# Kernel optimization log

Hardware: AMD Instinct MI355X
Metric: run time of the kernel (lower is better)

The kernel has to match this reference:

```python
import jax, jax.numpy as jnp
import numpy as np

B, S, D, H = 2, 2048, 1024, 16
DH = D // H  # 64


def setup_inputs() -> dict:
    key = jax.random.key(0)
    ks = jax.random.split(key, 12)
    scale = 0.02
    q = jax.random.normal(ks[0], (B, S, D), dtype=jnp.float32)
    k = jax.random.normal(ks[1], (B, S, D), dtype=jnp.float32)
    v = jax.random.normal(ks[2], (B, S, D), dtype=jnp.float32)
    # CTRL-style causal mask: 1.0 above the diagonal (positions to mask), 0.0 elsewhere
    mask = jnp.triu(jnp.ones((S, S), dtype=jnp.float32), k=1)
    Wq = jax.random.normal(ks[3], (D, D), dtype=jnp.float32) * scale
    bq = jnp.zeros((D,), dtype=jnp.float32)
    Wk = jax.random.normal(ks[4], (D, D), dtype=jnp.float32) * scale
    bk = jnp.zeros((D,), dtype=jnp.float32)
    Wv = jax.random.normal(ks[5], (D, D), dtype=jnp.float32) * scale
    bv = jnp.zeros((D,), dtype=jnp.float32)
    Wo = jax.random.normal(ks[6], (D, D), dtype=jnp.float32) * scale
    bo = jnp.zeros((D,), dtype=jnp.float32)
    return {"q": q, "k": k, "v": v, "mask": mask,
            "Wq": Wq, "bq": bq, "Wk": Wk, "bk": bk,
            "Wv": Wv, "bv": bv, "Wo": Wo, "bo": bo}


def _split_heads(x):
    # [B, S, D] -> [B, H, S, DH]
    b, s, _ = x.shape
    return x.reshape(b, s, H, DH).transpose(0, 2, 1, 3)


def reference(q, k, v, mask, Wq, bq, Wk, bk, Wv, bv, Wo, bo):
    # QKV projections
    qh = _split_heads(q @ Wq + bq)  # [B, H, S, DH]
    kh = _split_heads(k @ Wk + bk)
    vh = _split_heads(v @ Wv + bv)
    # scaled dot-product attention with CTRL mask convention (mask * -1e4 added)
    scores = jnp.einsum('bhqd,bhkd->bhqk', qh, kh) / jnp.sqrt(jnp.float32(DH))
    scores = scores + mask * -10000.0  # mask broadcasts [S,S] -> [B,H,S,S]
    weights = jax.nn.softmax(scores, axis=-1)
    ctx = jnp.einsum('bhqk,bhkd->bhqd', weights, vh)  # [B, H, S, DH]
    ctx = ctx.transpose(0, 2, 1, 3).reshape(q.shape[0], -1, D)  # [B, S, D]
    return ctx @ Wo + bo
```

## Files before the change

kernel.cpp:

```cpp
#include <hip/hip_runtime.h>
#include <stdint.h>

typedef unsigned short u16;
typedef __attribute__((ext_vector_type(8))) short bf16x8;
typedef __attribute__((ext_vector_type(4))) float f32x4;
typedef __attribute__((ext_vector_type(4))) unsigned short u16x4;

#define C_SCALE 0.1803368801111204f
#define C_MASK  -14426.950408889634f

__device__ __forceinline__ float bf2f(u16 x) {
  union { uint32_t u; float f; } v; v.u = ((uint32_t)x) << 16; return v.f;
}
__device__ __forceinline__ u16 f2bf(float f) {
  union { float f; uint32_t u; } v; v.f = f;
  return (u16)((v.u + 0x7FFFu + ((v.u >> 16) & 1u)) >> 16);
}

__device__ __forceinline__ void load_lds16(const void* g, void* l) {
  __builtin_amdgcn_global_load_lds(
      (const __attribute__((address_space(1))) uint32_t*)g,
      (__attribute__((address_space(3))) uint32_t*)l, 16, 0, 0);
}

__device__ __forceinline__ uint32_t pack_trunc(uint32_t f_even, uint32_t f_odd) {
  return __builtin_amdgcn_perm(f_odd, f_even, 0x07060302u);
}

__device__ __forceinline__ bool detect_bf16(const u16* __restrict__ q) {
  int lane = threadIdx.x & 63;
  u16 w = q[lane * 4];
  int e = (w >> 7) & 0xFF;
  unsigned long long b = __ballot(e >= 96 && e <= 159);
  return __popcll(b) >= 48;
}

__global__ __launch_bounds__(256) void transpose_all(const u16* __restrict__ W0,
                                                     const u16* __restrict__ W1,
                                                     const u16* __restrict__ W2,
                                                     const u16* __restrict__ W3,
                                                     u16* __restrict__ WTb,
                                                     const u16* __restrict__ qprobe) {
  constexpr int D = 1024;
  __shared__ u16 tile[64][72];
  const int z = blockIdx.z;
  const u16* W = z == 0 ? W0 : (z == 1 ? W1 : (z == 2 ? W2 : W3));
  u16* WT = WTb + (size_t)z * D * D;
  const bool isbf = detect_bf16(qprobe);
  const int x0 = blockIdx.x * 64, y0 = blockIdx.y * 64;
  const int t = threadIdx.x;
  const int r = t >> 3;
  const int c8 = (t & 7) << 3;
#pragma unroll
  for (int hh = 0; hh < 2; ++hh) {
    int row = r + hh * 32;
    if (isbf) {
      *(uint4*)&tile[row][c8] = *(const uint4*)&W[(size_t)(y0 + row) * D + x0 + c8];
    } else {
      const float* Wf = (const float*)W;
      float4 f0 = *(const float4*)&Wf[(size_t)(y0 + row) * D + x0 + c8];
      float4 f1 = *(const float4*)&Wf[(size_t)(y0 + row) * D + x0 + c8 + 4];
      u16 tmp[8] = {f2bf(f0.x), f2bf(f0.y), f2bf(f0.z), f2bf(f0.w),
                    f2bf(f1.x), f2bf(f1.y), f2bf(f1.z), f2bf(f1.w)};
      *(uint4*)&tile[row][c8] = *(uint4*)tmp;
    }
  }
  __syncthreads();
#pragma unroll
  for (int hh = 0; hh < 2; ++hh) {
    int row = r + hh * 32;
    u16 tmp[8];
#pragma unroll
    for (int i = 0; i < 8; ++i) tmp[i] = tile[c8 + i][row];
    *(uint4*)&WT[(size_t)(x0 + row) * D + y0 + c8] = *(uint4*)tmp;
  }
}

__global__ __launch_bounds__(256, 2) void gemm_qkv(
    const u16* __restrict__ A0, const u16* __restrict__ A1, const u16* __restrict__ A2,
    const u16* __restrict__ WTb,
    const u16* __restrict__ b0, const u16* __restrict__ b1, const u16* __restrict__ b2,
    u16* __restrict__ Chb) {
  constexpr int K = 1024;
  __shared__ u16 As[4][64 * 40];
  __shared__ u16 Bs[4][128 * 32];
  const int z = blockIdx.z;
  const u16* A = z == 0 ? A0 : (z == 1 ? A1 : A2);
  const u16* bias = z == 0 ? b0 : (z == 1 ? b1 : b2);
  const u16* BT = WTb + (size_t)z * 1024 * 1024;
  u16* C = Chb + (size_t)z * 4 * 1024 * 1024;
  const bool isbf = detect_bf16(A0);
  const int tid = threadIdx.x;
  const int wave = tid >> 6, lane = tid & 63;
  const int quad = lane >> 4, lr = lane & 15;
  const int f = blockIdx.x + 8 * blockIdx.y;
  const int n0 = (f >> 6) * 128;
  const int m0 = (f & 63) * 64;
  const int mW = (wave & 1) * 32, nW = (wave >> 1) * 64;
  const int ar = tid >> 2, ac = tid & 3;

  uint4 ra[2][2];
  auto loadA = [&](int t) {
    int slot = t & 1, k0 = t * 32;
    if (isbf) {
      ra[slot][0] = *(const uint4*)&A[(size_t)(m0 + ar) * K + k0 + ac * 8];
    } else {
      const uint32_t* Af = (const uint32_t*)A;
      ra[slot][0] = *(const uint4*)&Af[(size_t)(m0 + ar) * K + k0 + ac * 8];
      ra[slot][1] = *(const uint4*)&Af[(size_t)(m0 + ar) * K + k0 + ac * 8 + 4];
    }
  };
  auto writeA = [&](int t) {
    int slot = t & 1, buf = t & 3;
    if (isbf) {
      *(uint4*)&As[buf][ar * 40 + ac * 8] = ra[slot][0];
    } else {
      uint4 o;
      o.x = pack_trunc(ra[slot][0].x, ra[slot][0].y);
      o.y = pack_trunc(ra[slot][0].z, ra[slot][0].w);
      o.z = pack_trunc(ra[slot][1].x, ra[slot][1].y);
      o.w = pack_trunc(ra[slot][1].z, ra[slot][1].w);
      *(uint4*)&As[buf][ar * 40 + ac * 8] = o;
    }
  };
  auto stageB = [&](int t) {
    int buf = t & 3, k0 = t * 32;
#pragma unroll
    for (int p = 0; p < 2; ++p) {
      int s = (wave * 2 + p) * 64 + lane;
      int r = s >> 2, c = s & 3;
      int cg = c ^ (r & 3);
      load_lds16(&BT[(size_t)(n0 + r) * K + k0 + cg * 8],
                 &Bs[buf][(wave * 2 + p) * 512]);
    }
  };

  f32x4 acc[2][4] = {};

  loadA(0); loadA(1);
  stageB(0); stageB(1);
  writeA(0); writeA(1);
  loadA(2); loadA(3);
  __syncthreads();

  for (int j = 0; j < 16; ++j) {
    const int tc0 = 2 * j, tc1 = 2 * j + 1;
    if (tc0 + 2 < 32) {
      writeA(tc0 + 2); writeA(tc1 + 2);
      stageB(tc0 + 2); stageB(tc1 + 2);
      if (tc0 + 4 < 32) { loadA(tc0 + 4); loadA(tc1 + 4); }
    }
#pragma unroll
    for (int tt = 0; tt < 2; ++tt) {
      const int buf = (tc0 + tt) & 3;
      bf16x8 af[2], bfm[4];
#pragma unroll
      for (int i = 0; i < 2; ++i)
        af[i] = *(const bf16x8*)&As[buf][(mW + 16 * i + lr) * 40 + quad * 8];
#pragma unroll
      for (int jj = 0; jj < 4; ++jj) {
        int rr = nW + 16 * jj + lr;
        bfm[jj] = *(const bf16x8*)&Bs[buf][rr * 32 + ((quad ^ (rr & 3)) * 8)];
      }
#pragma unroll
      for (int i = 0; i < 2; ++i)
#pragma unroll
        for (int jj = 0; jj < 4; ++jj)
          acc[i][jj] =
              __builtin_amdgcn_mfma_f32_16x16x32_bf16(af[i], bfm[jj], acc[i][jj], 0, 0, 0);
    }
    __syncthreads();
  }

#pragma unroll
  for (int i = 0; i < 2; ++i) {
#pragma unroll
    for (int jj = 0; jj < 4; ++jj) {
      int n = n0 + nW + 16 * jj + lr;
      float bv = isbf ? bf2f(bias[n]) : ((const float*)bias)[n];
#pragma unroll
      for (int r = 0; r < 4; ++r) {
        int m = m0 + mW + 16 * i + quad * 4 + r;
        float val = acc[i][jj][r] + bv;
        int b = m >> 11, s = m & 2047, h = n >> 6, dh = n & 63;
        C[((size_t)(b * 16 + h) * 2048 + s) * 64 + dh] = f2bf(val);
      }
    }
  }
}

__global__ __launch_bounds__(256, 2) void gemm_out(const u16* __restrict__ A,
                                                   const u16* __restrict__ BT,
                                                   const u16* __restrict__ bias,
                                                   u16* __restrict__ C,
                                                   const u16* __restrict__ qprobe) {
  constexpr int K = 1024, N = 1024;
  __shared__ u16 As[4][64 * 32];
  __shared__ u16 Bs[4][128 * 32];
  const bool isbf = detect_bf16(qprobe);
  const int tid = threadIdx.x;
  const int wave = tid >> 6, lane = tid & 63;
  const int quad = lane >> 4, lr = lane & 15;
  const int f = blockIdx.x + 8 * blockIdx.y;
  const int n0 = (f >> 6) * 128;
  const int m0 = (f & 63) * 64;
  const int mW = (wave & 1) * 32, nW = (wave >> 1) * 64;

  auto stage = [&](int t) {
    int buf = t & 3, k0 = t * 32;
    {
      int s = wave * 64 + lane;
      int r = s >> 2, c = s & 3;
      int cg = c ^ (r & 3);
      load_lds16(&A[(size_t)(m0 + r) * K + k0 + cg * 8], &As[buf][wave * 512]);
    }
#pragma unroll
    for (int p = 0; p < 2; ++p) {
      int s = (wave * 2 + p) * 64 + lane;
      int r = s >> 2, c = s & 3;
      int cg = c ^ (r & 3);
      load_lds16(&BT[(size_t)(n0 + r) * K + k0 + cg * 8],
                 &Bs[buf][(wave * 2 + p) * 512]);
    }
  };

  f32x4 acc[2][4] = {};
  stage(0); stage(1);
  __syncthreads();

  for (int j = 0; j < 16; ++j) {
    const int tc0 = 2 * j;
    if (tc0 + 2 < 32) { stage(tc0 + 2); stage(tc0 + 3); }
#pragma unroll
    for (int tt = 0; tt < 2; ++tt) {
      const int buf = (tc0 + tt) & 3;
      bf16x8 af[2], bfm[4];
#pragma unroll
      for (int i = 0; i < 2; ++i) {
        int rr = mW + 16 * i + lr;
        af[i] = *(const bf16x8*)&As[buf][rr * 32 + ((quad ^ (rr & 3)) * 8)];
      }
#pragma unroll
      for (int jj = 0; jj < 4; ++jj) {
        int rr = nW + 16 * jj + lr;
        bfm[jj] = *(const bf16x8*)&Bs[buf][rr * 32 + ((quad ^ (rr & 3)) * 8)];
      }
#pragma unroll
      for (int i = 0; i < 2; ++i)
#pragma unroll
        for (int jj = 0; jj < 4; ++jj)
          acc[i][jj] =
              __builtin_amdgcn_mfma_f32_16x16x32_bf16(af[i], bfm[jj], acc[i][jj], 0, 0, 0);
    }
    __syncthreads();
  }

#pragma unroll
  for (int i = 0; i < 2; ++i) {
#pragma unroll
    for (int jj = 0; jj < 4; ++jj) {
      int n = n0 + nW + 16 * jj + lr;
      float bv = isbf ? bf2f(bias[n]) : ((const float*)bias)[n];
#pragma unroll
      for (int r = 0; r < 4; ++r) {
        int m = m0 + mW + 16 * i + quad * 4 + r;
        float val = acc[i][jj][r] + bv;
        size_t idx = (size_t)m * N + n;
        if (isbf) C[idx] = f2bf(val);
        else ((float*)C)[idx] = val;
      }
    }
  }
}

__global__ __launch_bounds__(256, 2) void attn_fwd(const u16* __restrict__ Qh,
                                                   const u16* __restrict__ Kh,
                                                   const u16* __restrict__ Vh,
                                                   u16* __restrict__ ctx) {
  constexpr int S = 2048, DH = 64, Dm = 1024;
  __shared__ u16 Ks[2][64 * 64];
  __shared__ u16 Vt[2][64 * 72];
  __shared__ u16 Pl[4][16 * 72];
  const int tid = threadIdx.x;
  const int wave = tid >> 6, lane = tid & 63;
  const int quad = lane >> 4, lr = lane & 15;
  const int bh = blockIdx.y;
  const int bx = (int)blockIdx.x;
  const size_t base = (size_t)bh * S * DH;
  const u16* Q = Qh + base;
  const u16* Kp = Kh + base;
  const u16* Vp = Vh + base;
  u16* Plw = Pl[wave];
  const int b = bh >> 4, h = bh & 15;

  const int vkey2 = (tid & 31) * 2, vd8 = (tid >> 5) * 8;
  uint4 va, vbr;

  auto stageK = [&](int kt, int kbuf) {
#pragma unroll
    for (int p = 0; p < 2; ++p) {
      int s = (wave * 2 + p) * 64 + lane;
      int r = s >> 3, cg = (s & 7) ^ (r & 7);
      load_lds16(&Kp[(size_t)(kt + r) * DH + cg * 8], &Ks[kbuf][(wave * 2 + p) * 512]);
    }
  };
  auto loadV = [&](int kt) {
    va  = *(const uint4*)&Vp[(size_t)(kt + vkey2) * DH + vd8];
    vbr = *(const uint4*)&Vp[(size_t)(kt + vkey2 + 1) * DH + vd8];
  };
  auto writeV = [&](int vbuf) {
    const u16* pa = (const u16*)&va;
    const u16* pb = (const u16*)&vbr;
#pragma unroll
    for (int i = 0; i < 8; ++i) {
      uint32_t pair = (uint32_t)pa[i] | ((uint32_t)pb[i] << 16);
      *(uint32_t*)&Vt[vbuf][(vd8 + i) * 72 + vkey2] = pair;
    }
  };

  int kb = 0, vb = 0;
  for (int ph = 0; ph < 2; ++ph) {
    const int qt = ph == 0 ? (31 - bx) : bx;
    const int q0 = qt * 64;
    const int nt = qt + 1;
    const int qg = q0 + wave * 16 + lr;

    bf16x8 aQ[2];
#pragma unroll
    for (int s = 0; s < 2; ++s)
      aQ[s] = *(const bf16x8*)&Q[(size_t)(q0 + wave * 16 + lr) * DH + s * 32 + quad * 8];

    f32x4 o[4] = {};
    float m_i = -1.0e5f;
    float l_i = 0.f;

    __syncthreads();
    stageK(0, kb);
    loadV(0);
    writeV(vb);
    if (nt > 1) loadV(64);

    for (int it = 0; it < nt; ++it) {
      const int kt = it * 64;
      __syncthreads();

      bf16x8 aK[4][2], bV[4][2];
#pragma unroll
      for (int t = 0; t < 4; ++t) {
        int r = t * 16 + lr;
#pragma unroll
        for (int s = 0; s < 2; ++s) {
          int ch = (s * 4 + quad) ^ (r & 7);
          aK[t][s] = *(const bf16x8*)&Ks[kb][r * 64 + ch * 8];
        }
      }
#pragma unroll
      for (int c = 0; c < 4; ++c)
#pragma unroll
        for (int s = 0; s < 2; ++s)
          bV[c][s] = *(const bf16x8*)&Vt[vb][(c * 16 + lr) * 72 + s * 32 + quad * 8];

      if (it + 1 < nt) {
        stageK(kt + 64, kb ^ 1);
        writeV(vb ^ 1);
        if (it + 2 < nt) loadV(kt + 128);
      }

      f32x4 sc[4];
#pragma unroll
      for (int t = 0; t < 4; ++t) {
        f32x4 zz = {0.f, 0.f, 0.f, 0.f};
        zz = __builtin_amdgcn_mfma_f32_16x16x32_bf16(aK[t][0], aQ[0], zz, 0, 0, 0);
        zz = __builtin_amdgcn_mfma_f32_16x16x32_bf16(aK[t][1], aQ[1], zz, 0, 0, 0);
        sc[t] = zz;
      }

      const bool diag = (it == nt - 1);
      float v[4][4];
      float mx = -1.0e5f;
      if (diag) {
#pragma unroll
        for (int t = 0; t < 4; ++t)
#pragma unroll
          for (int r = 0; r < 4; ++r) {
            int kg = kt + t * 16 + quad * 4 + r;
            float x = sc[t][r] * C_SCALE + ((kg > qg) ? C_MASK : 0.f);
            v[t][r] = x;
            mx = fmaxf(mx, x);
          }
      } else {
#pragma unroll
        for (int t = 0; t < 4; ++t)
#pragma unroll
          for (int r = 0; r < 4; ++r) {
            float x = sc[t][r] * C_SCALE;
            v[t][r] = x;
            mx = fmaxf(mx, x);
          }
      }
      mx = fmaxf(mx, __shfl_xor(mx, 16));
      mx = fmaxf(mx, __shfl_xor(mx, 32));
      float m_new = fmaxf(m_i, mx);
      float sum = 0.f;
      u16 pb16[4][4];
#pragma unroll
      for (int t = 0; t < 4; ++t)
#pragma unroll
        for (int r = 0; r < 4; ++r) {
          float p = exp2f(v[t][r] - m_new);
          sum += p;
          pb16[t][r] = f2bf(p);
        }
      sum += __shfl_xor(sum, 16);
      sum += __shfl_xor(sum, 32);
      float alpha = exp2f(m_i - m_new);
      l_i = l_i * alpha + sum;
      m_i = m_new;
#pragma unroll
      for (int t = 0; t < 4; ++t) {
        u16x4 w = {pb16[t][0], pb16[t][1], pb16[t][2], pb16[t][3]};
        *(u16x4*)&Plw[lr * 72 + t * 16 + quad * 4] = w;
      }
#pragma unroll
      for (int r = 0; r < 4; ++r) {
        float ab = __shfl(alpha, quad * 4 + r);
#pragma unroll
        for (int c = 0; c < 4; ++c) o[c][r] *= ab;
      }
      asm volatile("s_waitcnt lgkmcnt(0)" ::: "memory");
      bf16x8 aP[2];
#pragma unroll
      for (int s = 0; s < 2; ++s)
        aP[s] = *(const bf16x8*)&Plw[lr * 72 + s * 32 + quad * 8];
#pragma unroll
      for (int c = 0; c < 4; ++c)
#pragma unroll
        for (int s = 0; s < 2; ++s)
          o[c] = __builtin_amdgcn_mfma_f32_16x16x32_bf16(aP[s], bV[c][s], o[c], 0, 0, 0);
      kb ^= 1; vb ^= 1;
    }

    float linv = 1.f / l_i;
#pragma unroll
    for (int r = 0; r < 4; ++r) {
      float lb = __shfl(linv, quad * 4 + r);
      int s = q0 + wave * 16 + quad * 4 + r;
      size_t orow = ((size_t)b * S + s) * Dm + h * DH;
#pragma unroll
      for (int c = 0; c < 4; ++c) ctx[orow + c * 16 + lr] = f2bf(o[c][r] * lb);
    }
  }
}

extern "C" void kernel_launch(void* const* d_in, const int* in_sizes, int n_in,
                              void* d_out, int out_size, void* d_ws, size_t ws_size,
                              hipStream_t stream) {
  const u16* q  = (const u16*)d_in[0];
  const u16* k  = (const u16*)d_in[1];
  const u16* v  = (const u16*)d_in[2];
  const u16* Wq = (const u16*)d_in[4];
  const u16* bq = (const u16*)d_in[5];
  const u16* Wk = (const u16*)d_in[6];
  const u16* bk = (const u16*)d_in[7];
  const u16* Wv = (const u16*)d_in[8];
  const u16* bv = (const u16*)d_in[9];
  const u16* Wo = (const u16*)d_in[10];
  const u16* bo = (const u16*)d_in[11];
  u16* out = (u16*)d_out;

  constexpr size_t M1 = 1024 * 1024;
  u16* ws = (u16*)d_ws;
  u16* WT  = ws;
  u16* Qh  = WT + 4 * M1;
  u16* ctx = Qh + 12 * M1;

  dim3 tb(256);
  transpose_all<<<dim3(16, 16, 4), tb, 0, stream>>>(Wq, Wk, Wv, Wo, WT, q);
  gemm_qkv<<<dim3(8, 64, 3), tb, 0, stream>>>(q, k, v, WT, bq, bk, bv, Qh);
  attn_fwd<<<dim3(16, 32), tb, 0, stream>>>(Qh, Qh + 4 * M1, Qh + 8 * M1, ctx);
  gemm_out<<<dim3(8, 64), tb, 0, stream>>>(ctx, WT + 3 * M1, bo, out, q);
}
```

Before: 252.2 us.

## Rework projection GEMMs with 128x128 tiles and explicit multi-stage waitcnt pipelines

Both the QKV and output projection GEMMs move from 64x128 to 128x128 block tiles, so each wave now computes a 64x64 sub-tile with 16 MFMAs per k-step. The k-loop is rewritten as an N-stage ring buffer, 3 stages for QKV and 6 for the output GEMM, driven by manual s_waitcnt vmcnt counts, raw s_barrier and sched_barrier instead of __syncthreads. This is meant to raise data reuse per LDS read and keep global loads overlapping with compute. It adds a separate fp32-input path that converts A through registers, and it reduces the grid to 256 blocks per GEMM, which costs occupancy and relies on hand-tuned wait counts being correct.

```diff
diff --git a/kernel.cpp b/kernel.cpp
--- a/kernel.cpp
+++ b/kernel.cpp
@@ -34,6 +34,22 @@
   unsigned long long b = __ballot(e >= 96 && e <= 159);
   return __popcll(b) >= 48;
 }
+
+__device__ __forceinline__ void wait_vm(int n) {
+  switch (n) {
+    case 0:  __builtin_amdgcn_s_waitcnt(0x0F70); break;
+    case 2:  __builtin_amdgcn_s_waitcnt(0x0F72); break;
+    case 4:  __builtin_amdgcn_s_waitcnt(0x0F74); break;
+    case 6:  __builtin_amdgcn_s_waitcnt(0x0F76); break;
+    case 8:  __builtin_amdgcn_s_waitcnt(0x0F78); break;
+    case 12: __builtin_amdgcn_s_waitcnt(0x0F7C); break;
+    case 16: __builtin_amdgcn_s_waitcnt(0x4F70); break;
+    default: __builtin_amdgcn_s_waitcnt(0x4F74); break;
+  }
+}
+__device__ __forceinline__ void wait_lgkm0() { __builtin_amdgcn_s_waitcnt(0xC07F); }
+#define SBAR()  __builtin_amdgcn_s_barrier()
+#define SCHED() __builtin_amdgcn_sched_barrier(0)
 
 __global__ __launch_bounds__(256) void transpose_all(const u16* __restrict__ W0,
                                                      const u16* __restrict__ W1,
@@ -76,15 +92,177 @@
   }
 }
 
-__global__ __launch_bounds__(256, 2) void gemm_qkv(
+
+__device__ __forceinline__ void stage_tile32(const u16* __restrict__ src, int row0,
+                                             int k0, u16* dst, int wave, int lane) {
+  constexpr int K = 1024;
+#pragma unroll
+  for (int p = 0; p < 2; ++p) {
+    int seg = wave * 2 + p;
+    int r = seg * 16 + (lane >> 2);
+    int c = lane & 3;
+    int cg = c ^ (r & 3);
+    load_lds16(&src[(size_t)(row0 + r) * K + k0 + cg * 8], dst + seg * 512);
+  }
+}
+
+#define FRAG_READS(Ab, Bb)                                                    \
+  _Pragma("unroll") for (int i = 0; i < 4; ++i) {                             \
+    int r = wm + 16 * i + lr;                                                 \
+    af[i] = *(const bf16x8*)&(Ab)[r * 32 + ((quad ^ (r & 3)) * 8)];           \
+  }                                                                           \
+  _Pragma("unroll") for (int jj = 0; jj < 4; ++jj) {                          \
+    int r = wn + 16 * jj + lr;                                                \
+    bff[jj] = *(const bf16x8*)&(Bb)[r * 32 + ((quad ^ (r & 3)) * 8)];         \
+  }
+
+#define MFMA16()                                                              \
+  _Pragma("unroll") for (int i = 0; i < 4; ++i)                               \
+  _Pragma("unroll") for (int jj = 0; jj < 4; ++jj)                            \
+      acc[i][jj] = __builtin_amdgcn_mfma_f32_16x16x32_bf16(af[i], bff[jj],    \
+                                                           acc[i][jj], 0, 0, 0);
+
+template <int NS>
+__device__ __forceinline__ void kloop_dma(const u16* __restrict__ A,
+                                          const u16* __restrict__ BT,
+                                          int m0, int n0, u16* As, u16* Bs,
+                                          int wave, int lane, f32x4 (&acc)[4][4]) {
+  const int quad = lane >> 4, lr = lane & 15;
+  const int wm = (wave & 1) * 64, wn = (wave >> 1) * 64;
+  auto stage = [&](int t, int buf) {
+    stage_tile32(A, m0, t * 32, As + buf * 4096, wave, lane);
+    stage_tile32(BT, n0, t * 32, Bs + buf * 4096, wave, lane);
+  };
+#pragma unroll
+  for (int s = 0; s < NS; ++s) stage(s, s);
+  int buf = 0;
+#pragma unroll 1
+  for (int t = 0; t < 32; ++t) {
+    SCHED();
+    int rem = 31 - t;
+    wait_vm(rem >= NS - 1 ? 4 * (NS - 1) : 4 * rem);
+    SBAR();
+    SCHED();
+    bf16x8 af[4], bff[4];
+    const u16* Ab = As + buf * 4096;
+    const u16* Bb = Bs + buf * 4096;
+    FRAG_READS(Ab, Bb)
+    wait_lgkm0();
+    SCHED();
+    SBAR();
+    if (t + NS < 32) stage(t + NS, buf);
+    MFMA16()
+    buf = buf + 1 == NS ? 0 : buf + 1;
+  }
+}
+
+__device__ __forceinline__ void kloop_f32(const float* __restrict__ Af,
+                                          const u16* __restrict__ BT,
+                                          int m0, int n0, u16* As, u16* Bs,
+                                          int tid, f32x4 (&acc)[4][4]) {
+  constexpr int K = 1024;
+  const int wave = tid >> 6, lane = tid & 63;
+  const int quad = lane >> 4, lr = lane & 15;
+  const int wm = (wave & 1) * 64, wn = (wave >> 1) * 64;
+  const int ar = tid >> 1, ah = tid & 1;
+  const uint32_t* Au = (const uint32_t*)Af;
+  uint4 ra0[4], ra1[4];
+  auto loadA = [&](int t, uint4 (&r)[4]) {
+    const uint32_t* p = &Au[(size_t)(m0 + ar) * K + t * 32 + ah * 16];
+    r[0] = *(const uint4*)(p + 0);
+    r[1] = *(const uint4*)(p + 4);
+    r[2] = *(const uint4*)(p + 8);
+    r[3] = *(const uint4*)(p + 12);
+  };
+  auto writeA = [&](int buf, uint4 (&rr)[4]) {
+    uint4 o0, o1;
+    o0.x = pack_trunc(rr[0].x, rr[0].y); o0.y = pack_trunc(rr[0].z, rr[0].w);
+    o0.z = pack_trunc(rr[1].x, rr[1].y); o0.w = pack_trunc(rr[1].z, rr[1].w);
+    o1.x = pack_trunc(rr[2].x, rr[2].y); o1.y = pack_trunc(rr[2].z, rr[2].w);
+    o1.z = pack_trunc(rr[3].x, rr[3].y); o1.w = pack_trunc(rr[3].z, rr[3].w);
+    int c0 = 2 * ah, c1 = 2 * ah + 1;
+    *(uint4*)&As[buf * 4096 + ar * 32 + ((c0 ^ (ar & 3)) * 8)] = o0;
+    *(uint4*)&As[buf * 4096 + ar * 32 + ((c1 ^ (ar & 3)) * 8)] = o1;
+  };
+  auto stageB = [&](int t, int buf) {
+    stage_tile32(BT, n0, t * 32, Bs + buf * 4096, wave, lane);
+  };
+  stageB(0, 0); loadA(0, ra0);
+  stageB(1, 1); loadA(1, ra1);
+  SCHED(); wait_vm(6); writeA(0, ra0);
+  stageB(2, 2); loadA(2, ra0);
+  SCHED(); wait_vm(6); writeA(1, ra1);
+  loadA(3, ra1);
+  SCHED(); wait_vm(4); writeA(2, ra0);
+
+  int buf = 0;
+#pragma unroll 1
+  for (int j = 0; j < 14; ++j) {
+#pragma unroll
+    for (int half = 0; half < 2; ++half) {
+      const int t = 2 * j + half;
+      SCHED();
+      wait_vm(16);
+      SBAR();
+      SCHED();
+      bf16x8 af[4], bff[4];
+      const u16* Ab = As + buf * 4096;
+      const u16* Bb = Bs + buf * 4096;
+      FRAG_READS(Ab, Bb)
+      wait_lgkm0();
+      SCHED();
+      SBAR();
+      stageB(t + 3, buf);
+      if (half == 0) { loadA(t + 4, ra0); SCHED(); wait_vm(6); writeA(buf, ra1); }
+      else           { loadA(t + 4, ra1); SCHED(); wait_vm(6); writeA(buf, ra0); }
+      MFMA16()
+      buf = buf + 1 == 3 ? 0 : buf + 1;
+    }
+  }
+  {
+    SCHED(); wait_vm(16); SBAR(); SCHED();
+    bf16x8 af[4], bff[4];
+    const u16 *Ab = As + buf * 4096, *Bb = Bs + buf * 4096;
+    FRAG_READS(Ab, Bb)
+    wait_lgkm0(); SCHED(); SBAR();
+    stageB(31, buf);
+    SCHED(); wait_vm(2); writeA(buf, ra1);
+    MFMA16()
+    buf = 2;
+  }
+  {
+    SCHED(); wait_vm(12); SBAR(); SCHED();
+    bf16x8 af[4], bff[4];
+    const u16 *Ab = As + buf * 4096, *Bb = Bs + buf * 4096;
+    FRAG_READS(Ab, Bb)
+    MFMA16()
+    buf = 0;
+  }
+  {
+    SCHED(); wait_vm(6); SBAR(); SCHED();
+    bf16x8 af[4], bff[4];
+    const u16 *Ab = As + buf * 4096, *Bb = Bs + buf * 4096;
+    FRAG_READS(Ab, Bb)
+    MFMA16()
+    buf = 1;
+  }
+  {
+    SCHED(); wait_vm(0); SBAR(); SCHED();
+    bf16x8 af[4], bff[4];
+    const u16 *Ab = As + buf * 4096, *Bb = Bs + buf * 4096;
+    FRAG_READS(Ab, Bb)
+    MFMA16()
+  }
+}
+
+__global__ __launch_bounds__(256, 3) void gemm_qkv(
     const u16* __restrict__ A0, const u16* __restrict__ A1, const u16* __restrict__ A2,
     const u16* __restrict__ WTb,
     const u16* __restrict__ b0, const u16* __restrict__ b1, const u16* __restrict__ b2,
     u16* __restrict__ Chb) {
-  constexpr int K = 1024;
-  __shared__ u16 As[4][64 * 40];
-  __shared__ u16 Bs[4][128 * 32];
-  const int z = blockIdx.z;
+  __shared__ u16 As[3 * 4096];
+  __shared__ u16 Bs[3 * 4096];
+  const int z = blockIdx.y;
   const u16* A = z == 0 ? A0 : (z == 1 ? A1 : A2);
   const u16* bias = z == 0 ? b0 : (z == 1 ? b1 : b2);
   const u16* BT = WTb + (size_t)z * 1024 * 1024;
@@ -93,94 +271,24 @@
   const int tid = threadIdx.x;
   const int wave = tid >> 6, lane = tid & 63;
   const int quad = lane >> 4, lr = lane & 15;
-  const int f = blockIdx.x + 8 * blockIdx.y;
-  const int n0 = (f >> 6) * 128;
-  const int m0 = (f & 63) * 64;
-  const int mW = (wave & 1) * 32, nW = (wave >> 1) * 64;
-  const int ar = tid >> 2, ac = tid & 3;
-
-  uint4 ra[2][2];
-  auto loadA = [&](int t) {
-    int slot = t & 1, k0 = t * 32;
-    if (isbf) {
-      ra[slot][0] = *(const uint4*)&A[(size_t)(m0 + ar) * K + k0 + ac * 8];
-    } else {
-      const uint32_t* Af = (const uint32_t*)A;
-      ra[slot][0] = *(const uint4*)&Af[(size_t)(m0 + ar) * K + k0 + ac * 8];
-      ra[slot][1] = *(const uint4*)&Af[(size_t)(m0 + ar) * K + k0 + ac * 8 + 4];
-    }
-  };
-  auto writeA = [&](int t) {
-    int slot = t & 1, buf = t & 3;
-    if (isbf) {
-      *(uint4*)&As[buf][ar * 40 + ac * 8] = ra[slot][0];
-    } else {
-      uint4 o;
-      o.x = pack_trunc(ra[slot][0].x, ra[slot][0].y);
-      o.y = pack_trunc(ra[slot][0].z, ra[slot][0].w);
-      o.z = pack_trunc(ra[slot][1].x, ra[slot][1].y);
-      o.w = pack_trunc(ra[slot][1].z, ra[slot][1].w);
-      *(uint4*)&As[buf][ar * 40 + ac * 8] = o;
-    }
-  };
-  auto stageB = [&](int t) {
-    int buf = t & 3, k0 = t * 32;
-#pragma unroll
-    for (int p = 0; p < 2; ++p) {
-      int s = (wave * 2 + p) * 64 + lane;
-      int r = s >> 2, c = s & 3;
-      int cg = c ^ (r & 3);
-      load_lds16(&BT[(size_t)(n0 + r) * K + k0 + cg * 8],
-                 &Bs[buf][(wave * 2 + p) * 512]);
-    }
-  };
-
-  f32x4 acc[2][4] = {};
-
-  loadA(0); loadA(1);
-  stageB(0); stageB(1);
-  writeA(0); writeA(1);
-  loadA(2); loadA(3);
-  __syncthreads();
-
-  for (int j = 0; j < 16; ++j) {
-    const int tc0 = 2 * j, tc1 = 2 * j + 1;
-    if (tc0 + 2 < 32) {
-      writeA(tc0 + 2); writeA(tc1 + 2);
-      stageB(tc0 + 2); stageB(tc1 + 2);
-      if (tc0 + 4 < 32) { loadA(tc0 + 4); loadA(tc1 + 4); }
-    }
-#pragma unroll
-    for (int tt = 0; tt < 2; ++tt) {
-      const int buf = (tc0 + tt) & 3;
-      bf16x8 af[2], bfm[4];
-#pragma unroll
-      for (int i = 0; i < 2; ++i)
-        af[i] = *(const bf16x8*)&As[buf][(mW + 16 * i + lr) * 40 + quad * 8];
-#pragma unroll
-      for (int jj = 0; jj < 4; ++jj) {
-        int rr = nW + 16 * jj + lr;
-        bfm[jj] = *(const bf16x8*)&Bs[buf][rr * 32 + ((quad ^ (rr & 3)) * 8)];
-      }
-#pragma unroll
-      for (int i = 0; i < 2; ++i)
-#pragma unroll
-        for (int jj = 0; jj < 4; ++jj)
-          acc[i][jj] =
-              __builtin_amdgcn_mfma_f32_16x16x32_bf16(af[i], bfm[jj], acc[i][jj], 0, 0, 0);
-    }
-    __syncthreads();
-  }
-
-#pragma unroll
-  for (int i = 0; i < 2; ++i) {
+  const int f = blockIdx.x;
+  const int n0 = (f >> 5) * 128;
+  const int m0 = (f & 31) * 128;
+  const int wm = (wave & 1) * 64, wn = (wave >> 1) * 64;
+
+  f32x4 acc[4][4] = {};
+  if (isbf) kloop_dma<3>(A, BT, m0, n0, As, Bs, wave, lane, acc);
+  else      kloop_f32((const float*)A, BT, m0, n0, As, Bs, tid, acc);
+
+#pragma unroll
+  for (int i = 0; i < 4; ++i) {
 #pragma unroll
     for (int jj = 0; jj < 4; ++jj) {
-      int n = n0 + nW + 16 * jj + lr;
+      int n = n0 + wn + 16 * jj + lr;
       float bv = isbf ? bf2f(bias[n]) : ((const float*)bias)[n];
 #pragma unroll
       for (int r = 0; r < 4; ++r) {
-        int m = m0 + mW + 16 * i + quad * 4 + r;
+        int m = m0 + wm + 16 * i + quad * 4 + r;
         float val = acc[i][jj][r] + bv;
         int b = m >> 11, s = m & 2047, h = n >> 6, dh = n & 63;
         C[((size_t)(b * 16 + h) * 2048 + s) * 64 + dh] = f2bf(val);
@@ -189,81 +297,35 @@
   }
 }
 
-__global__ __launch_bounds__(256, 2) void gemm_out(const u16* __restrict__ A,
-                                                   const u16* __restrict__ BT,
-                                                   const u16* __restrict__ bias,
-                                                   u16* __restrict__ C,
-                                                   const u16* __restrict__ qprobe) {
-  constexpr int K = 1024, N = 1024;
-  __shared__ u16 As[4][64 * 32];
-  __shared__ u16 Bs[4][128 * 32];
+__global__ __launch_bounds__(256) void gemm_out(const u16* __restrict__ A,
+                                                const u16* __restrict__ BT,
+                                                const u16* __restrict__ bias,
+                                                u16* __restrict__ C,
+                                                const u16* __restrict__ qprobe) {
+  constexpr int N = 1024;
+  __shared__ u16 As[6 * 4096];
+  __shared__ u16 Bs[6 * 4096];
   const bool isbf = detect_bf16(qprobe);
   const int tid = threadIdx.x;
   const int wave = tid >> 6, lane = tid & 63;
   const int quad = lane >> 4, lr = lane & 15;
-  const int f = blockIdx.x + 8 * blockIdx.y;
-  const int n0 = (f >> 6) * 128;
-  const int m0 = (f & 63) * 64;
-  const int mW = (wave & 1) * 32, nW = (wave >> 1) * 64;
-
-  auto stage = [&](int t) {
-    int buf = t & 3, k0 = t * 32;
-    {
-      int s = wave * 64 + lane;
-      int r = s >> 2, c = s & 3;
-      int cg = c ^ (r & 3);
-      load_lds16(&A[(size_t)(m0 + r) * K + k0 + cg * 8], &As[buf][wave * 512]);
-    }
-#pragma unroll
-    for (int p = 0; p < 2; ++p) {
-      int s = (wave * 2 + p) * 64 + lane;
-      int r = s >> 2, c = s & 3;
-      int cg = c ^ (r & 3);
-      load_lds16(&BT[(size_t)(n0 + r) * K + k0 + cg * 8],
-                 &Bs[buf][(wave * 2 + p) * 512]);
-    }
-  };
-
-  f32x4 acc[2][4] = {};
-  stage(0); stage(1);
-  __syncthreads();
-
-  for (int j = 0; j < 16; ++j) {
-    const int tc0 = 2 * j;
-    if (tc0 + 2 < 32) { stage(tc0 + 2); stage(tc0 + 3); }
-#pragma unroll
-    for (int tt = 0; tt < 2; ++tt) {
-      const int buf = (tc0 + tt) & 3;
-      bf16x8 af[2], bfm[4];
-#pragma unroll
-      for (int i = 0; i < 2; ++i) {
-        int rr = mW + 16 * i + lr;
-        af[i] = *(const bf16x8*)&As[buf][rr * 32 + ((quad ^ (rr & 3)) * 8)];
-      }
-#pragma unroll
-      for (int jj = 0; jj < 4; ++jj) {
-        int rr = nW + 16 * jj + lr;
-        bfm[jj] = *(const bf16x8*)&Bs[buf][rr * 32 + ((quad ^ (rr & 3)) * 8)];
-      }
-#pragma unroll
-      for (int i = 0; i < 2; ++i)
-#pragma unroll
-        for (int jj = 0; jj < 4; ++jj)
-          acc[i][jj] =
-              __builtin_amdgcn_mfma_f32_16x16x32_bf16(af[i], bfm[jj], acc[i][jj], 0, 0, 0);
-    }
-    __syncthreads();
-  }
-
-#pragma unroll
-  for (int i = 0; i < 2; ++i) {
+  const int f = blockIdx.x;
+  const int n0 = (f >> 5) * 128;
+  const int m0 = (f & 31) * 128;
+  const int wm = (wave & 1) * 64, wn = (wave >> 1) * 64;
+
+  f32x4 acc[4][4] = {};
+  kloop_dma<6>(A, BT, m0, n0, As, Bs, wave, lane, acc);
+
+#pragma unroll
+  for (int i = 0; i < 4; ++i) {
 #pragma unroll
     for (int jj = 0; jj < 4; ++jj) {
-      int n = n0 + nW + 16 * jj + lr;
+      int n = n0 + wn + 16 * jj + lr;
       float bv = isbf ? bf2f(bias[n]) : ((const float*)bias)[n];
 #pragma unroll
       for (int r = 0; r < 4; ++r) {
-        int m = m0 + mW + 16 * i + quad * 4 + r;
+        int m = m0 + wm + 16 * i + quad * 4 + r;
         float val = acc[i][jj][r] + bv;
         size_t idx = (size_t)m * N + n;
         if (isbf) C[idx] = f2bf(val);
@@ -476,7 +538,7 @@
 
   dim3 tb(256);
   transpose_all<<<dim3(16, 16, 4), tb, 0, stream>>>(Wq, Wk, Wv, Wo, WT, q);
-  gemm_qkv<<<dim3(8, 64, 3), tb, 0, stream>>>(q, k, v, WT, bq, bk, bv, Qh);
+  gemm_qkv<<<dim3(256, 3), tb, 0, stream>>>(q, k, v, WT, bq, bk, bv, Qh);
   attn_fwd<<<dim3(16, 32), tb, 0, stream>>>(Qh, Qh + 4 * M1, Qh + 8 * M1, ctx);
-  gemm_out<<<dim3(8, 64), tb, 0, stream>>>(ctx, WT + 3 * M1, bo, out, q);
-}
+  gemm_out<<<dim3(256), tb, 0, stream>>>(ctx, WT + 3 * M1, bo, out, q);
+}
```

New measurement: 263.9 us. 4.6% more time.
